# Performance work log

Hardware: AMD Instinct MI355X
Metric: run time of the kernel (lower is better)

## Reference

```python
import jax, jax.numpy as jnp
import numpy as np

B, N = 16, 48
NODE, EDGE, HID, MSG, LAYERS, TGT = 32, 16, 64, 64, 3, 128
NL = 128  # hidden width of cfg.net_layers / cfg.layers MLPs


def _lin(key, i, o):
    k1, k2 = jax.random.split(key)
    return (jax.random.normal(k1, (i, o), jnp.float32) * 0.05,
            jax.random.normal(k2, (o,), jnp.float32) * 0.05)


def setup_inputs() -> dict:
    key = jax.random.key(0)
    ks = jax.random.split(key, 16)
    g = (jax.random.uniform(ks[0], (B, N, N)) < 0.5).astype(jnp.float32)
    h0 = jax.random.normal(ks[1], (B, N, NODE), jnp.float32)
    e = jax.random.normal(ks[2], (B, N, N, EDGE), jnp.float32)
    msg_w0, msg_b0 = _lin(ks[3], EDGE, NL)
    msg_w1, msg_b1 = _lin(ks[4], NL, NL)
    msg_w2, msg_b2 = _lin(ks[5], NL, MSG * HID)
    gru_wih = jax.random.normal(ks[6], (3 * HID, MSG), jnp.float32) * 0.05
    gru_whh = jax.random.normal(ks[7], (3 * HID, HID), jnp.float32) * 0.05
    gru_bih = jax.random.normal(ks[8], (3 * HID,), jnp.float32) * 0.05
    gru_bhh = jax.random.normal(ks[9], (3 * HID,), jnp.float32) * 0.05
    r0_w0, r0_b0 = _lin(ks[10], 2 * HID, NL)
    r0_w1, r0_b1 = _lin(ks[11], NL, NL)
    r0_w2, r0_b2 = _lin(ks[12], NL, TGT)
    r1_w0, r1_b0 = _lin(ks[13], HID, NL)
    r1_w1, r1_b1 = _lin(ks[14], NL, NL)
    r1_w2, r1_b2 = _lin(ks[15], NL, TGT)
    return dict(g=g, h0=h0, e=e,
                msg_w0=msg_w0, msg_b0=msg_b0, msg_w1=msg_w1, msg_b1=msg_b1,
                msg_w2=msg_w2, msg_b2=msg_b2,
                gru_wih=gru_wih, gru_whh=gru_whh, gru_bih=gru_bih, gru_bhh=gru_bhh,
                r0_w0=r0_w0, r0_b0=r0_b0, r0_w1=r0_w1, r0_b1=r0_b1, r0_w2=r0_w2, r0_b2=r0_b2,
                r1_w0=r1_w0, r1_b0=r1_b0, r1_w1=r1_w1, r1_b1=r1_b1, r1_w2=r1_w2, r1_b2=r1_b2)


def _net(x, w0, b0, w1, b1, w2, b2):
    # Net: relu hidden layers, linear output (matches torch Net with 2 hidden layers)
    x = jax.nn.relu(x @ w0 + b0)
    x = jax.nn.relu(x @ w1 + b1)
    return x @ w2 + b2


def _gru_step(x, h, wih, whh, bih, bhh):
    # torch.nn.GRU single step; gate order r, z, n
    gi = x @ wih.T + bih
    gh = h @ whh.T + bhh
    r = jax.nn.sigmoid(gi[:, :HID] + gh[:, :HID])
    z = jax.nn.sigmoid(gi[:, HID:2 * HID] + gh[:, HID:2 * HID])
    n = jnp.tanh(gi[:, 2 * HID:] + r * gh[:, 2 * HID:])
    return (1.0 - z) * n + z * h


def reference(g, h0, e,
              msg_w0, msg_b0, msg_w1, msg_b1, msg_w2, msg_b2,
              gru_wih, gru_whh, gru_bih, gru_bhh,
              r0_w0, r0_b0, r0_w1, r0_b1, r0_w2, r0_b2,
              r1_w0, r1_b0, r1_w1, r1_b1, r1_w2, r1_b2):
    # pad h0 up to hidden size
    h_first = jnp.concatenate(
        [h0, jnp.zeros((B, N, HID - NODE), h0.dtype)], axis=2)
    node_mask = (jnp.sum(h0, axis=2) > 0).astype(h0.dtype)[..., None]  # [B,N,1]

    # per-edge weight matrices from edge features (same every layer in the
    # original torch code, so compute once): [B*N*N, MSG, HID]
    m_w = _net(e.reshape(-1, EDGE), msg_w0, msg_b0, msg_w1, msg_b1,
               msg_w2, msg_b2).reshape(-1, MSG, HID)

    h_t = h_first
    for _ in range(LAYERS):
        h_feat = h_t.reshape(-1, HID)  # [B*N, HID]
        # faithful to torch: expand on last dim then view(-1, HID),
        # which interleaves the hidden and neighbor axes in memory order
        h_w_rows = jnp.broadcast_to(
            h_feat[:, :, None], (B * N, HID, N)).reshape(-1, HID)
        msg = jnp.einsum('emh,eh->em', m_w, h_w_rows)  # [B*N*N, MSG]
        msg = msg.reshape(B, N, N, MSG)
        agg = jnp.sum(g[..., None] * msg, axis=1)  # masked sum over dim 1 -> [B,N,MSG]
        h_new = _gru_step(agg.reshape(-1, MSG), h_t.reshape(-1, HID),
                          gru_wih, gru_whh, gru_bih, gru_bhh).reshape(B, N, HID)
        h_t = node_mask * h_new

    # readout: Net0(cat[h_0, h_T]) * Net1(h_T), masked by h_0 activity, summed over nodes
    gate_in = jnp.concatenate([h_first, h_t], axis=-1)  # [B,N,2*HID]
    nn_res = (_net(gate_in, r0_w0, r0_b0, r0_w1, r0_b1, r0_w2, r0_b2) *
              _net(h_t, r1_w0, r1_b0, r1_w1, r1_b1, r1_w2, r1_b2))  # [B,N,TGT]
    read_mask = (jnp.sum(h_first, axis=2) > 0).astype(nn_res.dtype)[..., None]
    res = jnp.sum(read_mask * nn_res, axis=1)  # [B,TGT]
    return jax.nn.sigmoid(res)
```

## Files before the change

kernel.cpp:

```cpp
#include <hip/hip_runtime.h>
#include <cmath>

#define B_ 16
#define N_ 48
#define HID_ 64
#define NL_ 128
#define NNODE_ (B_*N_)
#define NEDGE_ (B_*N_*N_)

__device__ __forceinline__ float sigmoidf_(float x){ return 1.0f/(1.0f+expf(-x)); }

__global__ void k_prep(const float* __restrict__ w2, const float* __restrict__ b2,
                       const float* __restrict__ h0,
                       const float* __restrict__ wih, const float* __restrict__ whh,
                       const float* __restrict__ w1,
                       float* __restrict__ A, float* __restrict__ Bm,
                       float* __restrict__ Ab, float* __restrict__ Bb,
                       float* __restrict__ hfirst, float* __restrict__ mask,
                       float* __restrict__ wihT, float* __restrict__ whhT,
                       float* __restrict__ w1T)
{
    int idx = blockIdx.x*256 + threadIdx.x;
    if (idx < 24576) {
        int r = idx >> 13;
        int c = (idx >> 6) & 127;
        int m = idx & 63;
        int t = 48 - 16*r;
        const float* src = w2 + c*4096 + m*64;
        float a = 0.f, b = 0.f;
        for (int k = 0; k < 64; k++){ float v = src[k]; if (k < t) a += v; else b += v; }
        A[idx] = a; Bm[idx] = b;
    } else if (idx < 24768) {
        int i2 = idx - 24576;
        int r = i2 >> 6, m = i2 & 63;
        int t = 48 - 16*r;
        const float* src = b2 + m*64;
        float a = 0.f, b = 0.f;
        for (int k = 0; k < 64; k++){ float v = src[k]; if (k < t) a += v; else b += v; }
        Ab[i2] = a; Bb[i2] = b;
    } else if (idx < 73920) {
        int i3 = idx - 24768;
        int node = i3 >> 6, m = i3 & 63;
        hfirst[i3] = (m < 32) ? h0[node*32 + m] : 0.f;
        if (m == 0) {
            float s = 0.f;
            for (int k = 0; k < 32; k++) s += h0[node*32 + k];
            mask[node] = (s > 0.f) ? 1.f : 0.f;
        }
    } else if (idx < 98496) {
        int i4 = idx - 73920;
        if (i4 < 12288) {
            int k = i4 / 192, col = i4 - k*192;
            wihT[i4] = wih[col*64 + k];
        } else {
            int i5 = i4 - 12288;
            int k = i5 / 192, col = i5 - k*192;
            whhT[i5] = whh[col*64 + k];
        }
    } else if (idx < 114880) {
        int i6 = idx - 98496;
        int o = i6 >> 7, i = i6 & 127;
        w1T[i6] = w1[i*128 + o];
    }
}

__global__ __launch_bounds__(256) void k_mlp(
    const float* __restrict__ ein, const float* __restrict__ w0, const float* __restrict__ b0,
    const float* __restrict__ w1T, const float* __restrict__ b1,
    float* __restrict__ relu2)
{
    __shared__ __align__(16) float x1s[64*132];
    int tid = threadIdx.x;
    int et = tid & 15, ot = tid >> 4;
    int o0 = ot * 8;
    size_t e0 = (size_t)blockIdx.x * 64;

    float acc[4][8];
    {
        float4 ba = *(const float4*)&b0[o0];
        float4 bb = *(const float4*)&b0[o0 + 4];
        #pragma unroll
        for (int q = 0; q < 4; q++){
            acc[q][0]=ba.x; acc[q][1]=ba.y; acc[q][2]=ba.z; acc[q][3]=ba.w;
            acc[q][4]=bb.x; acc[q][5]=bb.y; acc[q][6]=bb.z; acc[q][7]=bb.w;
        }
    }
    #pragma unroll
    for (int i4 = 0; i4 < 4; i4++){
        float4 ev[4];
        #pragma unroll
        for (int q = 0; q < 4; q++)
            ev[q] = *(const float4*)&ein[(e0 + q*16 + et)*16 + i4*4];
        #pragma unroll
        for (int d = 0; d < 4; d++){
            int i = i4*4 + d;
            float4 wa = *(const float4*)&w0[i*128 + o0];
            float4 wb = *(const float4*)&w0[i*128 + o0 + 4];
            #pragma unroll
            for (int q = 0; q < 4; q++){
                float xi = (d==0) ? ev[q].x : (d==1) ? ev[q].y : (d==2) ? ev[q].z : ev[q].w;
                acc[q][0] += xi*wa.x; acc[q][1] += xi*wa.y;
                acc[q][2] += xi*wa.z; acc[q][3] += xi*wa.w;
                acc[q][4] += xi*wb.x; acc[q][5] += xi*wb.y;
                acc[q][6] += xi*wb.z; acc[q][7] += xi*wb.w;
            }
        }
    }
    #pragma unroll
    for (int q = 0; q < 4; q++){
        int e = q*16 + et;
        float4 s0 = make_float4(fmaxf(acc[q][0],0.f), fmaxf(acc[q][1],0.f),
                                fmaxf(acc[q][2],0.f), fmaxf(acc[q][3],0.f));
        float4 s1 = make_float4(fmaxf(acc[q][4],0.f), fmaxf(acc[q][5],0.f),
                                fmaxf(acc[q][6],0.f), fmaxf(acc[q][7],0.f));
        *(float4*)&x1s[e*132 + o0]     = s0;
        *(float4*)&x1s[e*132 + o0 + 4] = s1;
    }
    __syncthreads();

    float a2[4][8];
    {
        float4 ba = *(const float4*)&b1[o0];
        float4 bb = *(const float4*)&b1[o0 + 4];
        #pragma unroll
        for (int q = 0; q < 4; q++){
            a2[q][0]=ba.x; a2[q][1]=ba.y; a2[q][2]=ba.z; a2[q][3]=ba.w;
            a2[q][4]=bb.x; a2[q][5]=bb.y; a2[q][6]=bb.z; a2[q][7]=bb.w;
        }
    }
    for (int i4 = 0; i4 < 32; i4++){
        int i = i4*4;
        float4 wv[8];
        #pragma unroll
        for (int r2 = 0; r2 < 8; r2++)
            wv[r2] = *(const float4*)&w1T[(size_t)(o0 + r2)*128 + i];
        #pragma unroll
        for (int q = 0; q < 4; q++){
            float4 xv = *(const float4*)&x1s[(q*16 + et)*132 + i];
            #pragma unroll
            for (int r2 = 0; r2 < 8; r2++){
                a2[q][r2] += xv.x*wv[r2].x + xv.y*wv[r2].y
                           + xv.z*wv[r2].z + xv.w*wv[r2].w;
            }
        }
    }
    #pragma unroll
    for (int q = 0; q < 4; q++){
        size_t e = e0 + q*16 + et;
        float4 s0 = make_float4(fmaxf(a2[q][0],0.f), fmaxf(a2[q][1],0.f),
                                fmaxf(a2[q][2],0.f), fmaxf(a2[q][3],0.f));
        float4 s1 = make_float4(fmaxf(a2[q][4],0.f), fmaxf(a2[q][5],0.f),
                                fmaxf(a2[q][6],0.f), fmaxf(a2[q][7],0.f));
        *(float4*)&relu2[e*128 + o0]     = s0;
        *(float4*)&relu2[e*128 + o0 + 4] = s1;
    }
}

__global__ __launch_bounds__(256) void k_layer(
    const float* __restrict__ hin, float* __restrict__ hout,
    const float* __restrict__ relu2,
    const float* __restrict__ A, const float* __restrict__ Bm,
    const float* __restrict__ Ab, const float* __restrict__ Bb,
    const float* __restrict__ g, const float* __restrict__ mask,
    const float* __restrict__ wihT, const float* __restrict__ whhT,
    const float* __restrict__ bih, const float* __restrict__ bhh)
{
    int bj = blockIdx.x;
    int b = bj / 48, j = bj - b*48;
    int r = j % 3;
    int p0 = j + j/3;
    int tid = threadIdx.x;
    int base = b*48;
    __shared__ float hs[64], wAs[48], wBs[48];
    __shared__ float pU[2][128], pV[2][128];
    __shared__ float Us[128], Vs[128];
    __shared__ float pC[4][64];
    __shared__ float sAB[2];
    __shared__ float aggs[64], gi[192], gh[192];

    if (tid < 64) hs[tid] = hin[(size_t)bj*64 + tid];
    else if (tid < 112){
        int i = tid - 64;
        int node = base + i;
        float gv = g[(size_t)node*48 + j];
        wAs[i] = gv * hin[(size_t)node*64 + p0];
        wBs[i] = gv * hin[(size_t)node*64 + p0 + 1];
    }
    __syncthreads();
    if (tid < 2){
        const float* src = tid ? wBs : wAs;
        float s = 0.f;
        for (int i = 0; i < 48; i++) s += src[i];
        sAB[tid] = s;
    }
    {
        int c = tid & 127, half = tid >> 7;
        const float* r2b = relu2 + ((size_t)base*48 + j)*128 + c;
        float aU = 0.f, aV = 0.f;
        for (int ii = 0; ii < 24; ii++){
            int i = half*24 + ii;
            float v = r2b[(size_t)i*6144];
            aU += wAs[i]*v; aV += wBs[i]*v;
        }
        pU[half][c] = aU; pV[half][c] = aV;
    }
    __syncthreads();
    if (tid < 128){ Us[tid] = pU[0][tid] + pU[1][tid]; Vs[tid] = pV[0][tid] + pV[1][tid]; }
    __syncthreads();
    {
        int m = tid & 63, cg = tid >> 6;
        const float* Arp = A  + r*8192 + m;
        const float* Brp = Bm + r*8192 + m;
        float a = 0.f;
        for (int cc = 0; cc < 32; cc++){
            int c = cg*32 + cc;
            a += Us[c]*Arp[c*64] + Vs[c]*Brp[c*64];
        }
        pC[cg][m] = a;
    }
    __syncthreads();
    if (tid < 64){
        aggs[tid] = pC[0][tid] + pC[1][tid] + pC[2][tid] + pC[3][tid]
                  + sAB[0]*Ab[r*64 + tid] + sAB[1]*Bb[r*64 + tid];
    }
    __syncthreads();
    if (tid < 192){
        float gacc = bih[tid], hacc = bhh[tid];
        for (int k = 0; k < 64; k++){
            gacc += aggs[k] * wihT[k*192 + tid];
            hacc += hs[k]   * whhT[k*192 + tid];
        }
        gi[tid] = gacc; gh[tid] = hacc;
    }
    __syncthreads();
    if (tid < 64){
        float rr = sigmoidf_(gi[tid] + gh[tid]);
        float zz = sigmoidf_(gi[64+tid] + gh[64+tid]);
        float nn = tanhf(gi[128+tid] + rr*gh[128+tid]);
        float hnew = (1.f - zz)*nn + zz*hs[tid];
        hout[(size_t)bj*64 + tid] = mask[bj] * hnew;
    }
}

__device__ __forceinline__ void rd_layer(
    const float* __restrict__ Xs, const float* __restrict__ W,
    const float* __restrict__ bias, float* __restrict__ Ys,
    int dim, int o, int ng, bool do_relu)
{
    float a0 = bias[o];
    float a1 = a0;
    for (int i = 0; i < dim; i += 4){
        float w0 = W[(size_t)(i+0)*128 + o];
        float w1 = W[(size_t)(i+1)*128 + o];
        float w2 = W[(size_t)(i+2)*128 + o];
        float w3 = W[(size_t)(i+3)*128 + o];
        const float4 x0 = *(const float4*)&Xs[ng*128 + i];
        const float4 x1 = *(const float4*)&Xs[(ng+2)*128 + i];
        a0 += x0.x*w0 + x0.y*w1 + x0.z*w2 + x0.w*w3;
        a1 += x1.x*w0 + x1.y*w1 + x1.z*w2 + x1.w*w3;
    }
    if (do_relu){ a0 = fmaxf(a0, 0.f); a1 = fmaxf(a1, 0.f); }
    Ys[ng*128 + o] = a0;
    Ys[(ng+2)*128 + o] = a1;
}

__global__ __launch_bounds__(256) void k_read(
    const float* __restrict__ hfirst, const float* __restrict__ hT,
    const float* __restrict__ mask,
    const float* __restrict__ w00, const float* __restrict__ b00,
    const float* __restrict__ w01, const float* __restrict__ b01,
    const float* __restrict__ w02, const float* __restrict__ b02,
    const float* __restrict__ w10, const float* __restrict__ b10,
    const float* __restrict__ w11, const float* __restrict__ b11,
    const float* __restrict__ w12, const float* __restrict__ b12,
    float* __restrict__ partial)
{
    __shared__ __align__(16) float xs[4*128];
    __shared__ __align__(16) float ys[4*128];
    __shared__ __align__(16) float zs[4*128];
    __shared__ __align__(16) float os0[4*128];
    __shared__ float mS[4];
    int tid = threadIdx.x;
    int b = blockIdx.x / 12, gg = blockIdx.x - b*12;
    int node0 = b*48 + gg*4;
    int o = tid & 127, ng = tid >> 7;
    if (tid < 4) mS[tid] = mask[node0 + tid];
    for (int i = tid; i < 4*128; i += 256){
        int r = i >> 7, c = i & 127;
        xs[i] = (c < 64) ? hfirst[(size_t)(node0+r)*64 + c]
                         : hT[(size_t)(node0+r)*64 + (c - 64)];
    }
    __syncthreads();
    rd_layer(xs,      w00, b00, ys,  128, o, ng, true);  __syncthreads();
    rd_layer(ys,      w01, b01, zs,  128, o, ng, true);  __syncthreads();
    rd_layer(zs,      w02, b02, os0, 128, o, ng, false); __syncthreads();
    rd_layer(xs + 64, w10, b10, ys,  64,  o, ng, true);  __syncthreads();
    rd_layer(ys,      w11, b11, zs,  128, o, ng, true);  __syncthreads();
    {
        float a0 = b12[o];
        float a1 = a0;
        for (int i = 0; i < 128; i += 4){
            float w0 = w12[(size_t)(i+0)*128 + o];
            float w1 = w12[(size_t)(i+1)*128 + o];
            float w2 = w12[(size_t)(i+2)*128 + o];
            float w3 = w12[(size_t)(i+3)*128 + o];
            const float4 x0 = *(const float4*)&zs[ng*128 + i];
            const float4 x1 = *(const float4*)&zs[(ng+2)*128 + i];
            a0 += x0.x*w0 + x0.y*w1 + x0.z*w2 + x0.w*w3;
            a1 += x1.x*w0 + x1.y*w1 + x1.z*w2 + x1.w*w3;
        }
        float s = mS[ng]   * os0[ng*128 + o]     * a0
                + mS[ng+2] * os0[(ng+2)*128 + o] * a1;
        __syncthreads();
        ys[ng*128 + o] = s;
    }
    __syncthreads();
    if (tid < 128)
        partial[(size_t)blockIdx.x*128 + tid] = ys[tid] + ys[128 + tid];
}

__global__ void k_final(const float* __restrict__ partial, float* __restrict__ out)
{
    int idx = blockIdx.x*256 + threadIdx.x;
    if (idx < B_*128){
        int b = idx >> 7, t = idx & 127;
        float s = 0.f;
        for (int c = 0; c < 12; c++) s += partial[(size_t)(b*12 + c)*128 + t];
        out[idx] = 1.0f / (1.0f + expf(-s));
    }
}

extern "C" void kernel_launch(void* const* d_in, const int* in_sizes, int n_in,
                              void* d_out, int out_size, void* d_ws, size_t ws_size,
                              hipStream_t stream)
{
    (void)in_sizes; (void)n_in; (void)out_size; (void)ws_size;
    const float* g    = (const float*)d_in[0];
    const float* h0   = (const float*)d_in[1];
    const float* e    = (const float*)d_in[2];
    const float* mw0  = (const float*)d_in[3];
    const float* mb0  = (const float*)d_in[4];
    const float* mw1  = (const float*)d_in[5];
    const float* mb1  = (const float*)d_in[6];
    const float* mw2  = (const float*)d_in[7];
    const float* mb2  = (const float*)d_in[8];
    const float* wih  = (const float*)d_in[9];
    const float* whh  = (const float*)d_in[10];
    const float* bih  = (const float*)d_in[11];
    const float* bhh  = (const float*)d_in[12];
    const float* r0w0 = (const float*)d_in[13];
    const float* r0b0 = (const float*)d_in[14];
    const float* r0w1 = (const float*)d_in[15];
    const float* r0b1 = (const float*)d_in[16];
    const float* r0w2 = (const float*)d_in[17];
    const float* r0b2 = (const float*)d_in[18];
    const float* r1w0 = (const float*)d_in[19];
    const float* r1b0 = (const float*)d_in[20];
    const float* r1w1 = (const float*)d_in[21];
    const float* r1b1 = (const float*)d_in[22];
    const float* r1w2 = (const float*)d_in[23];
    const float* r1b2 = (const float*)d_in[24];
    float* out = (float*)d_out;

    float* ws     = (float*)d_ws;
    float* A      = ws;
    float* Bm     = A      + 24576;
    float* Ab     = Bm     + 24576;
    float* Bb     = Ab     + 192;
    float* hfirst = Bb     + 192;
    float* hA     = hfirst + 49152;
    float* hB     = hA     + 49152;
    float* mask   = hB     + 49152;
    float* wihT   = mask   + 768;
    float* whhT   = wihT   + 12288;
    float* w1T    = whhT   + 12288;
    float* part   = w1T    + 16384;
    float* relu2  = part   + 24576;

    k_prep<<<449, 256, 0, stream>>>(mw2, mb2, h0, wih, whh, mw1,
                                    A, Bm, Ab, Bb, hfirst, mask, wihT, whhT, w1T);
    k_mlp<<<576, 256, 0, stream>>>(e, mw0, mb0, w1T, mb1, relu2);
    k_layer<<<768, 256, 0, stream>>>(hfirst, hA, relu2, A, Bm, Ab, Bb, g, mask,
                                     wihT, whhT, bih, bhh);
    k_layer<<<768, 256, 0, stream>>>(hA, hB, relu2, A, Bm, Ab, Bb, g, mask,
                                     wihT, whhT, bih, bhh);
    k_layer<<<768, 256, 0, stream>>>(hB, hA, relu2, A, Bm, Ab, Bb, g, mask,
                                     wihT, whhT, bih, bhh);
    k_read<<<192, 256, 0, stream>>>(hfirst, hA, mask,
                                    r0w0, r0b0, r0w1, r0b1, r0w2, r0b2,
                                    r1w0, r1b0, r1w1, r1b1, r1w2, r1b2, part);
    k_final<<<8, 256, 0, stream>>>(part, out);
}
```

Measured before the change: 193.6 us.

## Merge prep and edge MLP kernels, stage relu2 tile in shared memory

Folds the preparation kernel into the edge-MLP kernel as extra blocks, so one launch and its dependency edge go away. The w1 transpose is dropped and the second MLP layer now reads w1 row-major with an outer-product style accumulation. In the layer kernel, the 48x128 relu2 slice is loaded cooperatively into shared memory with float4 loads. The wA/wB sums now use a wavefront shuffle reduction, and the Ab/Bb vectors are staged in shared memory. Several loops gain unroll pragmas, at the cost of more shared memory per layer block, which may lower occupancy.

```diff
diff --git a/kernel.cpp b/kernel.cpp
--- a/kernel.cpp
+++ b/kernel.cpp
@@ -10,149 +10,153 @@
 
 __device__ __forceinline__ float sigmoidf_(float x){ return 1.0f/(1.0f+expf(-x)); }
 
-__global__ void k_prep(const float* __restrict__ w2, const float* __restrict__ b2,
-                       const float* __restrict__ h0,
-                       const float* __restrict__ wih, const float* __restrict__ whh,
-                       const float* __restrict__ w1,
-                       float* __restrict__ A, float* __restrict__ Bm,
-                       float* __restrict__ Ab, float* __restrict__ Bb,
-                       float* __restrict__ hfirst, float* __restrict__ mask,
-                       float* __restrict__ wihT, float* __restrict__ whhT,
-                       float* __restrict__ w1T)
-{
-    int idx = blockIdx.x*256 + threadIdx.x;
-    if (idx < 24576) {
-        int r = idx >> 13;
-        int c = (idx >> 6) & 127;
-        int m = idx & 63;
-        int t = 48 - 16*r;
-        const float* src = w2 + c*4096 + m*64;
-        float a = 0.f, b = 0.f;
-        for (int k = 0; k < 64; k++){ float v = src[k]; if (k < t) a += v; else b += v; }
-        A[idx] = a; Bm[idx] = b;
-    } else if (idx < 24768) {
-        int i2 = idx - 24576;
-        int r = i2 >> 6, m = i2 & 63;
-        int t = 48 - 16*r;
-        const float* src = b2 + m*64;
-        float a = 0.f, b = 0.f;
-        for (int k = 0; k < 64; k++){ float v = src[k]; if (k < t) a += v; else b += v; }
-        Ab[i2] = a; Bb[i2] = b;
-    } else if (idx < 73920) {
-        int i3 = idx - 24768;
-        int node = i3 >> 6, m = i3 & 63;
-        hfirst[i3] = (m < 32) ? h0[node*32 + m] : 0.f;
-        if (m == 0) {
-            float s = 0.f;
-            for (int k = 0; k < 32; k++) s += h0[node*32 + k];
-            mask[node] = (s > 0.f) ? 1.f : 0.f;
-        }
-    } else if (idx < 98496) {
-        int i4 = idx - 73920;
-        if (i4 < 12288) {
-            int k = i4 / 192, col = i4 - k*192;
-            wihT[i4] = wih[col*64 + k];
-        } else {
-            int i5 = i4 - 12288;
-            int k = i5 / 192, col = i5 - k*192;
-            whhT[i5] = whh[col*64 + k];
-        }
-    } else if (idx < 114880) {
-        int i6 = idx - 98496;
-        int o = i6 >> 7, i = i6 & 127;
-        w1T[i6] = w1[i*128 + o];
-    }
-}
-
-__global__ __launch_bounds__(256) void k_mlp(
+__global__ __launch_bounds__(256) void k_pm(
     const float* __restrict__ ein, const float* __restrict__ w0, const float* __restrict__ b0,
-    const float* __restrict__ w1T, const float* __restrict__ b1,
-    float* __restrict__ relu2)
+    const float* __restrict__ w1, const float* __restrict__ b1,
+    const float* __restrict__ w2, const float* __restrict__ b2,
+    const float* __restrict__ h0,
+    const float* __restrict__ wih, const float* __restrict__ whh,
+    float* __restrict__ relu2,
+    float* __restrict__ A, float* __restrict__ Bm,
+    float* __restrict__ Ab, float* __restrict__ Bb,
+    float* __restrict__ hfirst, float* __restrict__ mask,
+    float* __restrict__ wihT, float* __restrict__ whhT)
 {
     __shared__ __align__(16) float x1s[64*132];
     int tid = threadIdx.x;
-    int et = tid & 15, ot = tid >> 4;
-    int o0 = ot * 8;
-    size_t e0 = (size_t)blockIdx.x * 64;
-
-    float acc[4][8];
-    {
-        float4 ba = *(const float4*)&b0[o0];
-        float4 bb = *(const float4*)&b0[o0 + 4];
+
+    if (blockIdx.x < 576){
+        int et = tid & 15, ot = tid >> 4;
+        int o0 = ot * 8;
+        size_t e0 = (size_t)blockIdx.x * 64;
+
+        float acc[4][8];
+        {
+            float4 ba = *(const float4*)&b0[o0];
+            float4 bb = *(const float4*)&b0[o0 + 4];
+            #pragma unroll
+            for (int q = 0; q < 4; q++){
+                acc[q][0]=ba.x; acc[q][1]=ba.y; acc[q][2]=ba.z; acc[q][3]=ba.w;
+                acc[q][4]=bb.x; acc[q][5]=bb.y; acc[q][6]=bb.z; acc[q][7]=bb.w;
+            }
+        }
+        #pragma unroll
+        for (int i4 = 0; i4 < 4; i4++){
+            float4 ev[4];
+            #pragma unroll
+            for (int q = 0; q < 4; q++)
+                ev[q] = *(const float4*)&ein[(e0 + q*16 + et)*16 + i4*4];
+            float wr[4][8];
+            #pragma unroll
+            for (int d = 0; d < 4; d++){
+                *(float4*)&wr[d][0] = *(const float4*)&w0[(i4*4+d)*128 + o0];
+                *(float4*)&wr[d][4] = *(const float4*)&w0[(i4*4+d)*128 + o0 + 4];
+            }
+            #pragma unroll
+            for (int q = 0; q < 4; q++){
+                #pragma unroll
+                for (int r2 = 0; r2 < 8; r2++)
+                    acc[q][r2] += ev[q].x*wr[0][r2] + ev[q].y*wr[1][r2]
+                                + ev[q].z*wr[2][r2] + ev[q].w*wr[3][r2];
+            }
+        }
         #pragma unroll
         for (int q = 0; q < 4; q++){
-            acc[q][0]=ba.x; acc[q][1]=ba.y; acc[q][2]=ba.z; acc[q][3]=ba.w;
-            acc[q][4]=bb.x; acc[q][5]=bb.y; acc[q][6]=bb.z; acc[q][7]=bb.w;
-        }
-    }
-    #pragma unroll
-    for (int i4 = 0; i4 < 4; i4++){
-        float4 ev[4];
-        #pragma unroll
-        for (int q = 0; q < 4; q++)
-            ev[q] = *(const float4*)&ein[(e0 + q*16 + et)*16 + i4*4];
-        #pragma unroll
-        for (int d = 0; d < 4; d++){
-            int i = i4*4 + d;
-            float4 wa = *(const float4*)&w0[i*128 + o0];
-            float4 wb = *(const float4*)&w0[i*128 + o0 + 4];
+            int e = q*16 + et;
+            float4 s0 = make_float4(fmaxf(acc[q][0],0.f), fmaxf(acc[q][1],0.f),
+                                    fmaxf(acc[q][2],0.f), fmaxf(acc[q][3],0.f));
+            float4 s1 = make_float4(fmaxf(acc[q][4],0.f), fmaxf(acc[q][5],0.f),
+                                    fmaxf(acc[q][6],0.f), fmaxf(acc[q][7],0.f));
+            *(float4*)&x1s[e*132 + o0]     = s0;
+            *(float4*)&x1s[e*132 + o0 + 4] = s1;
+        }
+        __syncthreads();
+
+        float a2[4][8];
+        {
+            float4 ba = *(const float4*)&b1[o0];
+            float4 bb = *(const float4*)&b1[o0 + 4];
             #pragma unroll
             for (int q = 0; q < 4; q++){
-                float xi = (d==0) ? ev[q].x : (d==1) ? ev[q].y : (d==2) ? ev[q].z : ev[q].w;
-                acc[q][0] += xi*wa.x; acc[q][1] += xi*wa.y;
-                acc[q][2] += xi*wa.z; acc[q][3] += xi*wa.w;
-                acc[q][4] += xi*wb.x; acc[q][5] += xi*wb.y;
-                acc[q][6] += xi*wb.z; acc[q][7] += xi*wb.w;
-            }
-        }
-    }
-    #pragma unroll
-    for (int q = 0; q < 4; q++){
-        int e = q*16 + et;
-        float4 s0 = make_float4(fmaxf(acc[q][0],0.f), fmaxf(acc[q][1],0.f),
-                                fmaxf(acc[q][2],0.f), fmaxf(acc[q][3],0.f));
-        float4 s1 = make_float4(fmaxf(acc[q][4],0.f), fmaxf(acc[q][5],0.f),
-                                fmaxf(acc[q][6],0.f), fmaxf(acc[q][7],0.f));
-        *(float4*)&x1s[e*132 + o0]     = s0;
-        *(float4*)&x1s[e*132 + o0 + 4] = s1;
-    }
-    __syncthreads();
-
-    float a2[4][8];
-    {
-        float4 ba = *(const float4*)&b1[o0];
-        float4 bb = *(const float4*)&b1[o0 + 4];
+                a2[q][0]=ba.x; a2[q][1]=ba.y; a2[q][2]=ba.z; a2[q][3]=ba.w;
+                a2[q][4]=bb.x; a2[q][5]=bb.y; a2[q][6]=bb.z; a2[q][7]=bb.w;
+            }
+        }
+        for (int i4 = 0; i4 < 32; i4++){
+            int i = i4*4;
+            float wr[4][8];
+            #pragma unroll
+            for (int d = 0; d < 4; d++){
+                *(float4*)&wr[d][0] = *(const float4*)&w1[(size_t)(i+d)*128 + o0];
+                *(float4*)&wr[d][4] = *(const float4*)&w1[(size_t)(i+d)*128 + o0 + 4];
+            }
+            #pragma unroll
+            for (int q = 0; q < 4; q++){
+                float4 xv = *(const float4*)&x1s[(q*16 + et)*132 + i];
+                #pragma unroll
+                for (int r2 = 0; r2 < 8; r2++)
+                    a2[q][r2] += xv.x*wr[0][r2] + xv.y*wr[1][r2]
+                               + xv.z*wr[2][r2] + xv.w*wr[3][r2];
+            }
+        }
         #pragma unroll
         for (int q = 0; q < 4; q++){
-            a2[q][0]=ba.x; a2[q][1]=ba.y; a2[q][2]=ba.z; a2[q][3]=ba.w;
-            a2[q][4]=bb.x; a2[q][5]=bb.y; a2[q][6]=bb.z; a2[q][7]=bb.w;
-        }
-    }
-    for (int i4 = 0; i4 < 32; i4++){
-        int i = i4*4;
-        float4 wv[8];
-        #pragma unroll
-        for (int r2 = 0; r2 < 8; r2++)
-            wv[r2] = *(const float4*)&w1T[(size_t)(o0 + r2)*128 + i];
-        #pragma unroll
-        for (int q = 0; q < 4; q++){
-            float4 xv = *(const float4*)&x1s[(q*16 + et)*132 + i];
-            #pragma unroll
-            for (int r2 = 0; r2 < 8; r2++){
-                a2[q][r2] += xv.x*wv[r2].x + xv.y*wv[r2].y
-                           + xv.z*wv[r2].z + xv.w*wv[r2].w;
-            }
-        }
-    }
-    #pragma unroll
-    for (int q = 0; q < 4; q++){
-        size_t e = e0 + q*16 + et;
-        float4 s0 = make_float4(fmaxf(a2[q][0],0.f), fmaxf(a2[q][1],0.f),
-                                fmaxf(a2[q][2],0.f), fmaxf(a2[q][3],0.f));
-        float4 s1 = make_float4(fmaxf(a2[q][4],0.f), fmaxf(a2[q][5],0.f),
-                                fmaxf(a2[q][6],0.f), fmaxf(a2[q][7],0.f));
-        *(float4*)&relu2[e*128 + o0]     = s0;
-        *(float4*)&relu2[e*128 + o0 + 4] = s1;
+            size_t e = e0 + q*16 + et;
+            float4 s0 = make_float4(fmaxf(a2[q][0],0.f), fmaxf(a2[q][1],0.f),
+                                    fmaxf(a2[q][2],0.f), fmaxf(a2[q][3],0.f));
+            float4 s1 = make_float4(fmaxf(a2[q][4],0.f), fmaxf(a2[q][5],0.f),
+                                    fmaxf(a2[q][6],0.f), fmaxf(a2[q][7],0.f));
+            *(float4*)&relu2[e*128 + o0]     = s0;
+            *(float4*)&relu2[e*128 + o0 + 4] = s1;
+        }
+    } else {
+        int idx = (blockIdx.x - 576)*256 + tid;
+        if (idx < 24576) {
+            int r = idx >> 13, c = (idx >> 6) & 127, m = idx & 63;
+            int t = 48 - 16*r;
+            const float* src = w2 + c*4096 + m*64;
+            float a = 0.f, b = 0.f;
+            #pragma unroll
+            for (int k4 = 0; k4 < 16; k4++){
+                float4 v = *(const float4*)&src[k4*4];
+                float s = v.x + v.y + v.z + v.w;
+                if (k4*4 < t) a += s; else b += s;
+            }
+            A[idx] = a; Bm[idx] = b;
+        } else if (idx < 24768) {
+            int i2 = idx - 24576;
+            int r = i2 >> 6, m = i2 & 63;
+            int t = 48 - 16*r;
+            const float* src = b2 + m*64;
+            float a = 0.f, b = 0.f;
+            #pragma unroll
+            for (int k4 = 0; k4 < 16; k4++){
+                float4 v = *(const float4*)&src[k4*4];
+                float s = v.x + v.y + v.z + v.w;
+                if (k4*4 < t) a += s; else b += s;
+            }
+            Ab[i2] = a; Bb[i2] = b;
+        } else if (idx < 73920) {
+            int i3 = idx - 24768;
+            int node = i3 >> 6, m = i3 & 63;
+            hfirst[i3] = (m < 32) ? h0[node*32 + m] : 0.f;
+            if (m == 0) {
+                float s = 0.f;
+                #pragma unroll
+                for (int k = 0; k < 32; k++) s += h0[node*32 + k];
+                mask[node] = (s > 0.f) ? 1.f : 0.f;
+            }
+        } else if (idx < 98496) {
+            int i4 = idx - 73920;
+            if (i4 < 12288) {
+                int k = i4 / 192, col = i4 - k*192;
+                wihT[i4] = wih[col*64 + k];
+            } else {
+                int i5 = i4 - 12288;
+                int k = i5 / 192, col = i5 - k*192;
+                whhT[i5] = whh[col*64 + k];
+            }
+        }
     }
 }
 
@@ -171,61 +175,86 @@
     int p0 = j + j/3;
     int tid = threadIdx.x;
     int base = b*48;
-    __shared__ float hs[64], wAs[48], wBs[48];
+    __shared__ __align__(16) float r2s[48*128];
+    __shared__ float hs[64], wAs[64], wBs[64], Abs[64], Bbs[64];
     __shared__ float pU[2][128], pV[2][128];
-    __shared__ float Us[128], Vs[128];
     __shared__ float pC[4][64];
+    __shared__ float aggs[64], gi[192], gh[192];
     __shared__ float sAB[2];
-    __shared__ float aggs[64], gi[192], gh[192];
-
-    if (tid < 64) hs[tid] = hin[(size_t)bj*64 + tid];
-    else if (tid < 112){
+
+    {
+        const float* src = relu2 + ((size_t)base*48 + j)*128;
+        #pragma unroll
+        for (int q2 = 0; q2 < 6; q2++){
+            int flat = q2*256 + tid;
+            int row = flat >> 5, col = (flat & 31)*4;
+            float4 v = *(const float4*)&src[(size_t)row*6144 + col];
+            *(float4*)&r2s[row*128 + col] = v;
+        }
+    }
+    if (tid < 64){
+        hs[tid] = hin[(size_t)bj*64 + tid];
+    } else if (tid < 128){
         int i = tid - 64;
-        int node = base + i;
-        float gv = g[(size_t)node*48 + j];
-        wAs[i] = gv * hin[(size_t)node*64 + p0];
-        wBs[i] = gv * hin[(size_t)node*64 + p0 + 1];
-    }
-    __syncthreads();
-    if (tid < 2){
-        const float* src = tid ? wBs : wAs;
-        float s = 0.f;
-        for (int i = 0; i < 48; i++) s += src[i];
-        sAB[tid] = s;
-    }
+        float wa = 0.f, wb = 0.f;
+        if (i < 48){
+            float gv = g[(size_t)(base+i)*48 + j];
+            wa = gv * hin[(size_t)(base+i)*64 + p0];
+            wb = gv * hin[(size_t)(base+i)*64 + p0 + 1];
+        }
+        wAs[i] = wa; wBs[i] = wb;
+        float sa = wa, sb = wb;
+        #pragma unroll
+        for (int d = 32; d >= 1; d >>= 1){
+            sa += __shfl_xor(sa, d, 64);
+            sb += __shfl_xor(sb, d, 64);
+        }
+        if (i == 0){ sAB[0] = sa; sAB[1] = sb; }
+    } else if (tid < 192){
+        Bbs[tid-128] = Bb[r*64 + (tid-128)];
+    } else {
+        Abs[tid-192] = Ab[r*64 + (tid-192)];
+    }
+    __syncthreads();
+
     {
         int c = tid & 127, half = tid >> 7;
-        const float* r2b = relu2 + ((size_t)base*48 + j)*128 + c;
         float aU = 0.f, aV = 0.f;
+        #pragma unroll
         for (int ii = 0; ii < 24; ii++){
             int i = half*24 + ii;
-            float v = r2b[(size_t)i*6144];
+            float v = r2s[i*128 + c];
             aU += wAs[i]*v; aV += wBs[i]*v;
         }
         pU[half][c] = aU; pV[half][c] = aV;
     }
     __syncthreads();
-    if (tid < 128){ Us[tid] = pU[0][tid] + pU[1][tid]; Vs[tid] = pV[0][tid] + pV[1][tid]; }
-    __syncthreads();
+
     {
         int m = tid & 63, cg = tid >> 6;
         const float* Arp = A  + r*8192 + m;
         const float* Brp = Bm + r*8192 + m;
         float a = 0.f;
+        #pragma unroll
         for (int cc = 0; cc < 32; cc++){
             int c = cg*32 + cc;
-            a += Us[c]*Arp[c*64] + Vs[c]*Brp[c*64];
+            float u = pU[0][c] + pU[1][c];
+            float v = pV[0][c] + pV[1][c];
+            a += u*Arp[(size_t)c*64] + v*Brp[(size_t)c*64];
         }
         pC[cg][m] = a;
     }
     __syncthreads();
+
     if (tid < 64){
         aggs[tid] = pC[0][tid] + pC[1][tid] + pC[2][tid] + pC[3][tid]
-                  + sAB[0]*Ab[r*64 + tid] + sAB[1]*Bb[r*64 + tid];
-    }
-    __syncthreads();
+                  + sAB[0]*Abs[tid] + sAB[1]*Bbs[tid];
+    }
+    __syncthreads();
+
     if (tid < 192){
         float gacc = bih[tid], hacc = bhh[tid];
+        #pragma unroll 16
         for (int k = 0; k < 64; k++){
             gacc += aggs[k] * wihT[k*192 + tid];
             hacc += hs[k]   * whhT[k*192 + tid];
@@ -233,6 +262,7 @@
         gi[tid] = gacc; gh[tid] = hacc;
     }
     __syncthreads();
+
     if (tid < 64){
         float rr = sigmoidf_(gi[tid] + gh[tid]);
         float zz = sigmoidf_(gi[64+tid] + gh[64+tid]);
@@ -249,6 +279,7 @@
 {
     float a0 = bias[o];
     float a1 = a0;
+    #pragma unroll 8
     for (int i = 0; i < dim; i += 4){
         float w0 = W[(size_t)(i+0)*128 + o];
         float w1 = W[(size_t)(i+1)*128 + o];
@@ -299,6 +330,7 @@
     {
         float a0 = b12[o];
         float a1 = a0;
+        #pragma unroll 8
         for (int i = 0; i < 128; i += 4){
             float w0 = w12[(size_t)(i+0)*128 + o];
             float w1 = w12[(size_t)(i+1)*128 + o];
@@ -325,6 +357,7 @@
     if (idx < B_*128){
         int b = idx >> 7, t = idx & 127;
         float s = 0.f;
+        #pragma unroll
         for (int c = 0; c < 12; c++) s += partial[(size_t)(b*12 + c)*128 + t];
         out[idx] = 1.0f / (1.0f + expf(-s));
     }
@@ -373,13 +406,11 @@
     float* mask   = hB     + 49152;
     float* wihT   = mask   + 768;
     float* whhT   = wihT   + 12288;
-    float* w1T    = whhT   + 12288;
-    float* part   = w1T    + 16384;
+    float* part   = whhT   + 12288;
     float* relu2  = part   + 24576;
 
-    k_prep<<<449, 256, 0, stream>>>(mw2, mb2, h0, wih, whh, mw1,
-                                    A, Bm, Ab, Bb, hfirst, mask, wihT, whhT, w1T);
-    k_mlp<<<576, 256, 0, stream>>>(e, mw0, mb0, w1T, mb1, relu2);
+    k_pm<<<961, 256, 0, stream>>>(e, mw0, mb0, mw1, mb1, mw2, mb2, h0, wih, whh,
+                                  relu2, A, Bm, Ab, Bb, hfirst, mask, wihT, whhT);
     k_layer<<<768, 256, 0, stream>>>(hfirst, hA, relu2, A, Bm, Ab, Bb, g, mask,
                                      wihT, whhT, bih, bhh);
     k_layer<<<768, 256, 0, stream>>>(hA, hB, relu2, A, Bm, Ab, Bb, g, mask,
```

Result: slower. 209.9 us (+8.4%).
